# Optimization experiments

Hardware: AMD Instinct MI355X
Metric: run time of the kernel (lower is better)

## Reference

```python
import jax, jax.numpy as jnp
import numpy as np

B, T, H = 4, 2048, 512
HEADS = 8
D = H // HEADS  # head dim = 64


def setup_inputs() -> dict:
    key = jax.random.key(0)
    ks = jax.random.split(key, 5)
    s = 1.0 / np.sqrt(H)
    return {
        "x": jax.random.normal(ks[0], (B, T, H), dtype=jnp.float32),
        "w_qkv": jax.random.uniform(ks[1], (H, 3 * H), dtype=jnp.float32, minval=-s, maxval=s),
        "b_qkv": jax.random.uniform(ks[2], (3 * H,), dtype=jnp.float32, minval=-s, maxval=s),
        "w_proj": jax.random.uniform(ks[3], (H, H), dtype=jnp.float32, minval=-s, maxval=s),
        "b_proj": jax.random.uniform(ks[4], (H,), dtype=jnp.float32, minval=-s, maxval=s),
    }


def reference(x, w_qkv, b_qkv, w_proj, b_proj):
    b, t, h = x.shape
    scale = (h // HEADS) ** (-0.5)
    qkv = (x @ w_qkv + b_qkv).reshape(b, t, 3, HEADS, h // HEADS)
    q, k, v = qkv[:, :, 0], qkv[:, :, 1], qkv[:, :, 2]  # [b,t,heads,d]
    q = q * scale
    scores = jnp.einsum('bthd,bThd->bhtT', q, k)  # [b,heads,t,t]
    weights = jax.nn.softmax(scores, axis=-1)
    attn = jnp.einsum('bhtT,bThd->bthd', weights, v).reshape(b, t, h)
    return attn @ w_proj + b_proj
```

## Files before the change

### kernel.cpp

```cpp
#include <hip/hip_runtime.h>
#include <stdint.h>

typedef unsigned short u16;
typedef __attribute__((ext_vector_type(8))) __bf16 bf16x8;
typedef __attribute__((ext_vector_type(4))) __bf16 bf16x4;
typedef __attribute__((ext_vector_type(4))) float f32x4;
typedef __attribute__((ext_vector_type(2))) unsigned int u32x2;
typedef __attribute__((ext_vector_type(4))) unsigned int u32x4;

#define QSCALE 0.18033688011112042f

__device__ __forceinline__ u16 f2bf(float f) {
    uint32_t u = __builtin_bit_cast(uint32_t, f);
    u = (u + 0x7fffu + ((u >> 16) & 1u)) >> 16;
    return (u16)u;
}
__device__ __forceinline__ float bf2f(u16 h) {
    uint32_t u = ((uint32_t)h) << 16;
    return __builtin_bit_cast(float, u);
}

__device__ __forceinline__ void gl_lds16(const u16* g, u16* l) {
    __builtin_amdgcn_global_load_lds(
        (__attribute__((address_space(1))) uint32_t*)(g),
        (__attribute__((address_space(3))) uint32_t*)(l), 16, 0, 0);
}

__global__ __launch_bounds__(256) void convert_x_k(const float* __restrict__ xf,
                                                   u16* __restrict__ xbf) {
    const size_t v = (size_t)blockIdx.x * 256 + threadIdx.x;
    const f32x4 val = ((const f32x4*)xf)[v];
    u32x2 p;
    p.x = (uint32_t)f2bf(val.x) | ((uint32_t)f2bf(val.y) << 16);
    p.y = (uint32_t)f2bf(val.z) | ((uint32_t)f2bf(val.w) << 16);
    *(u32x2*)&xbf[v * 4] = p;
}

__global__ void transpose_cvt_k(const float* __restrict__ in,
                                u16* __restrict__ out, int R, int C) {
    __shared__ u16 t[64][65];
    const int bx = blockIdx.x << 6, by = blockIdx.y << 6;
    const int tx = threadIdx.x, ty = threadIdx.y;
#pragma unroll
    for (int i = ty; i < 64; i += 8)
        t[i][tx] = f2bf(in[(size_t)(by + i) * C + bx + tx]);
    __syncthreads();
#pragma unroll
    for (int i = ty; i < 64; i += 8) out[(size_t)(bx + i) * R + by + tx] = t[tx][i];
}

template <int EPI>
__global__ __launch_bounds__(256) void gemm_bt_k(
    const u16* __restrict__ A, const u16* __restrict__ Bt,
    const float* __restrict__ bias,
    u16* __restrict__ Qb, u16* __restrict__ Kb, u16* __restrict__ Vt,
    float* __restrict__ OutF) {
    __shared__ u16 lA[128 * 32];
    __shared__ u16 lB[128 * 32];
    const int tid = threadIdx.x;
    const int w = tid >> 6, l = tid & 63, quad = l >> 4, r = l & 15;
    const int tm = blockIdx.x << 7, tn = blockIdx.y << 7;
    const int wm = (w >> 1) << 6, wn = (w & 1) << 6;
    const int srow = l >> 2, sch = (l & 3) << 3;

    f32x4 acc[4][4];
#pragma unroll
    for (int i = 0; i < 4; ++i)
#pragma unroll
        for (int j = 0; j < 4; ++j) acc[i][j] = (f32x4){0.f, 0.f, 0.f, 0.f};

    for (int kk = 0; kk < 512; kk += 32) {
        __syncthreads();
#pragma unroll
        for (int ii = 0; ii < 2; ++ii) {
            const int rowl = w * 32 + ii * 16;
            gl_lds16(A + (size_t)(tm + rowl + srow) * 512 + kk + sch, &lA[rowl * 32]);
            gl_lds16(Bt + (size_t)(tn + rowl + srow) * 512 + kk + sch, &lB[rowl * 32]);
        }
        __syncthreads();
        bf16x8 af[4], bfr[4];
#pragma unroll
        for (int mi = 0; mi < 4; ++mi)
            af[mi] = *(const bf16x8*)&lA[(wm + mi * 16 + r) * 32 + quad * 8];
#pragma unroll
        for (int ni = 0; ni < 4; ++ni)
            bfr[ni] = *(const bf16x8*)&lB[(wn + ni * 16 + r) * 32 + quad * 8];
#pragma unroll
        for (int mi = 0; mi < 4; ++mi)
#pragma unroll
            for (int ni = 0; ni < 4; ++ni)
                acc[mi][ni] = __builtin_amdgcn_mfma_f32_16x16x32_bf16(
                    af[mi], bfr[ni], acc[mi][ni], 0, 0, 0);
    }

#pragma unroll
    for (int ni = 0; ni < 4; ++ni) {
        const int n = tn + wn + ni * 16 + r;
        const float bv = bias[n];
        const int which = n >> 9, head = (n >> 6) & 7, d = n & 63;
#pragma unroll
        for (int mi = 0; mi < 4; ++mi) {
#pragma unroll
            for (int i = 0; i < 4; ++i) {
                const int m = tm + wm + mi * 16 + quad * 4 + i;
                const float v = acc[mi][ni][i] + bv;
                if (EPI == 0) {
                    const int bb = m >> 11, t = m & 2047;
                    const int bh = bb * 8 + head;
                    if (which == 0)
                        Qb[((size_t)(bh * 2048 + t) << 6) + d] = f2bf(v * QSCALE);
                    else if (which == 1)
                        Kb[((size_t)(bh * 2048 + t) << 6) + d] = f2bf(v);
                    else
                        Vt[((size_t)(bh * 64 + d) << 11) + t] = f2bf(v);
                } else {
                    OutF[(size_t)m * 512 + n] = v;
                }
            }
        }
    }
}

__global__ __launch_bounds__(256) void attn_k(
    const u16* __restrict__ Qb, const u16* __restrict__ Kb,
    const u16* __restrict__ Vt, u16* __restrict__ attnb) {
    __shared__ u16 lk[64 * 64];
    __shared__ u16 lv[64 * 64];
    __shared__ u16 lp[4][16 * 72];
    const int tid = threadIdx.x;
    const int w = tid >> 6, l = tid & 63, quad = l >> 4, r = l & 15;
    const int qt = blockIdx.x, bh = blockIdx.y;
    const size_t qbase = (size_t)bh * 2048 + qt * 64;
    const int srl = l >> 3;
    const int sg = (l & 7) ^ srl;

    const bf16x8 qf0 = *(const bf16x8*)&Qb[((qbase + w * 16 + r) << 6) + quad * 8];
    const bf16x8 qf1 = *(const bf16x8*)&Qb[((qbase + w * 16 + r) << 6) + 32 + quad * 8];

    const int rl = r & 7;
    const int rhi = r >> 3;

    const u32x4 onesu = {0x3F803F80u, 0x3F803F80u, 0x3F803F80u, 0x3F803F80u};
    const bf16x8 vones = __builtin_bit_cast(bf16x8, onesu);

    f32x4 o[4];
#pragma unroll
    for (int i = 0; i < 4; ++i) o[i] = (f32x4){0.f, 0.f, 0.f, 0.f};
    f32x4 osum = (f32x4){0.f, 0.f, 0.f, 0.f};

    for (int kv0 = 0; kv0 < 2048; kv0 += 64) {
        __syncthreads();
#pragma unroll
        for (int ii = 0; ii < 2; ++ii) {
            const int chunk = w * 2 + ii;
            gl_lds16(Kb + ((size_t)(bh * 2048 + kv0 + chunk * 8 + srl) << 6) + sg * 8,
                     &lk[chunk * 512]);
            gl_lds16(Vt + (((size_t)(bh * 64 + chunk * 8 + srl)) << 11) + kv0 + sg * 8,
                     &lv[chunk * 512]);
        }
        __syncthreads();

#pragma unroll
        for (int kt = 0; kt < 4; ++kt) {
            const int base = (kt * 2 + rhi) * 512 + rl * 64;
            const bf16x8 a0 = *(const bf16x8*)&lk[base + (quad ^ rl) * 8];
            const bf16x8 a1 = *(const bf16x8*)&lk[base + ((quad ^ rl) ^ 4) * 8];
            f32x4 z = (f32x4){0.f, 0.f, 0.f, 0.f};
            z = __builtin_amdgcn_mfma_f32_16x16x32_bf16(a0, qf0, z, 0, 0, 0);
            z = __builtin_amdgcn_mfma_f32_16x16x32_bf16(a1, qf1, z, 0, 0, 0);
            const uint32_t u0 =
                __builtin_bit_cast(uint32_t, __builtin_amdgcn_exp2f(z[0])) + 0x8000u;
            const uint32_t u1 =
                __builtin_bit_cast(uint32_t, __builtin_amdgcn_exp2f(z[1])) + 0x8000u;
            const uint32_t u2 =
                __builtin_bit_cast(uint32_t, __builtin_amdgcn_exp2f(z[2])) + 0x8000u;
            const uint32_t u3 =
                __builtin_bit_cast(uint32_t, __builtin_amdgcn_exp2f(z[3])) + 0x8000u;
            const uint32_t lo = __builtin_amdgcn_perm(u1, u0, 0x07060302u);
            const uint32_t hi = __builtin_amdgcn_perm(u3, u2, 0x07060302u);
            const uint64_t both = (uint64_t)lo | ((uint64_t)hi << 32);
            *(bf16x4*)&lp[w][r * 72 + kt * 16 + quad * 4] =
                __builtin_bit_cast(bf16x4, both);
        }

        asm volatile("s_waitcnt lgkmcnt(0)" ::: "memory");

#pragma unroll
        for (int h = 0; h < 2; ++h) {
            const bf16x8 ap = *(const bf16x8*)&lp[w][r * 72 + h * 32 + quad * 8];
#pragma unroll
            for (int dt = 0; dt < 4; ++dt) {
                const int baseV = (dt * 2 + rhi) * 512 + rl * 64;
                const bf16x8 bv =
                    *(const bf16x8*)&lv[baseV + ((h * 4 + quad) ^ rl) * 8];
                o[dt] = __builtin_amdgcn_mfma_f32_16x16x32_bf16(ap, bv, o[dt], 0, 0, 0);
            }
            osum = __builtin_amdgcn_mfma_f32_16x16x32_bf16(ap, vones, osum, 0, 0, 0);
        }
    }

    const int bb = bh >> 3, head = bh & 7;
#pragma unroll
    for (int i = 0; i < 4; ++i) {
        const float inv = __builtin_amdgcn_rcpf(osum[i]);
        const int row = bb * 2048 + qt * 64 + w * 16 + quad * 4 + i;
#pragma unroll
        for (int dt = 0; dt < 4; ++dt)
            attnb[(size_t)row * 512 + head * 64 + dt * 16 + r] = f2bf(o[dt][i] * inv);
    }
}

extern "C" void kernel_launch(void* const* d_in, const int* in_sizes, int n_in,
                              void* d_out, int out_size, void* d_ws, size_t ws_size,
                              hipStream_t stream) {
    const float *x = nullptr, *wq = nullptr, *bq = nullptr, *wp = nullptr, *bp = nullptr;
    for (int i = 0; i < n_in; ++i) {
        switch (in_sizes[i]) {
            case 4194304: x  = (const float*)d_in[i]; break;
            case 786432:  wq = (const float*)d_in[i]; break;
            case 1536:    bq = (const float*)d_in[i]; break;
            case 262144:  wp = (const float*)d_in[i]; break;
            case 512:     bp = (const float*)d_in[i]; break;
        }
    }
    if (!x || !wq || !bq || !wp || !bp) {
        x = (const float*)d_in[0]; wq = (const float*)d_in[1];
        bq = (const float*)d_in[2]; wp = (const float*)d_in[3];
        bp = (const float*)d_in[4];
    }
    float* out = (float*)d_out;

    char* ws = (char*)d_ws;
    u16* attnb  = (u16*)(ws + 0);
    u16* wqkvT  = (u16*)(ws + 0);
    u16* Qb     = (u16*)(ws + 8388608);
    u16* wprojT = (u16*)(ws + 8388608);
    u16* Kb     = (u16*)(ws + 16777216);
    u16* Vt     = (u16*)(ws + 25165824);
    u16* xbf    = (u16*)d_out;

    convert_x_k<<<dim3(4096), 256, 0, stream>>>(x, xbf);
    transpose_cvt_k<<<dim3(24, 8), dim3(64, 8), 0, stream>>>(wq, wqkvT, 512, 1536);
    gemm_bt_k<0><<<dim3(64, 12), 256, 0, stream>>>(xbf, wqkvT, bq, Qb, Kb, Vt, nullptr);
    attn_k<<<dim3(32, 32), 256, 0, stream>>>(Qb, Kb, Vt, attnb);
    transpose_cvt_k<<<dim3(8, 8), dim3(64, 8), 0, stream>>>(wp, wprojT, 512, 512);
    gemm_bt_k<1><<<dim3(64, 4), 256, 0, stream>>>(attnb, wprojT, bp, nullptr, nullptr,
                                                  nullptr, out);
}
```

Before: 177.9 us.

## Process two 64-row query tiles per attention block to reuse K/V tiles

Each attention workgroup now handles 128 query rows instead of 64, with each wave holding two sets of Q fragments, accumulators and P buffers. Every K/V tile staged in LDS is used for twice as many MFMAs, which halves global K/V traffic and the number of barriers per unit of work. The cost is more registers and LDS per block, and the grid shrinks from 1024 to 512 blocks, which lowers the number of blocks available to fill the CUs.

Result: no change. 178.0 us (+0.1%).

```diff
diff --git a/kernel.cpp b/kernel.cpp
--- a/kernel.cpp
+++ b/kernel.cpp
@@ -126,16 +126,18 @@
     const u16* __restrict__ Vt, u16* __restrict__ attnb) {
     __shared__ u16 lk[64 * 64];
     __shared__ u16 lv[64 * 64];
-    __shared__ u16 lp[4][16 * 72];
+    __shared__ u16 lp[8][16 * 72];
     const int tid = threadIdx.x;
     const int w = tid >> 6, l = tid & 63, quad = l >> 4, r = l & 15;
     const int qt = blockIdx.x, bh = blockIdx.y;
-    const size_t qbase = (size_t)bh * 2048 + qt * 64;
+    const size_t qbase = (size_t)bh * 2048 + qt * 128;
     const int srl = l >> 3;
     const int sg = (l & 7) ^ srl;
 
-    const bf16x8 qf0 = *(const bf16x8*)&Qb[((qbase + w * 16 + r) << 6) + quad * 8];
-    const bf16x8 qf1 = *(const bf16x8*)&Qb[((qbase + w * 16 + r) << 6) + 32 + quad * 8];
+    const bf16x8 qf0a = *(const bf16x8*)&Qb[((qbase + w * 16 + r) << 6) + quad * 8];
+    const bf16x8 qf1a = *(const bf16x8*)&Qb[((qbase + w * 16 + r) << 6) + 32 + quad * 8];
+    const bf16x8 qf0b = *(const bf16x8*)&Qb[((qbase + 64 + w * 16 + r) << 6) + quad * 8];
+    const bf16x8 qf1b = *(const bf16x8*)&Qb[((qbase + 64 + w * 16 + r) << 6) + 32 + quad * 8];
 
     const int rl = r & 7;
     const int rhi = r >> 3;
@@ -143,10 +145,14 @@
     const u32x4 onesu = {0x3F803F80u, 0x3F803F80u, 0x3F803F80u, 0x3F803F80u};
     const bf16x8 vones = __builtin_bit_cast(bf16x8, onesu);
 
-    f32x4 o[4];
-#pragma unroll
-    for (int i = 0; i < 4; ++i) o[i] = (f32x4){0.f, 0.f, 0.f, 0.f};
-    f32x4 osum = (f32x4){0.f, 0.f, 0.f, 0.f};
+    f32x4 oA[4], oB[4];
+#pragma unroll
+    for (int i = 0; i < 4; ++i) {
+        oA[i] = (f32x4){0.f, 0.f, 0.f, 0.f};
+        oB[i] = (f32x4){0.f, 0.f, 0.f, 0.f};
+    }
+    f32x4 osumA = (f32x4){0.f, 0.f, 0.f, 0.f};
+    f32x4 osumB = (f32x4){0.f, 0.f, 0.f, 0.f};
 
     for (int kv0 = 0; kv0 < 2048; kv0 += 64) {
         __syncthreads();
@@ -165,48 +171,66 @@
             const int base = (kt * 2 + rhi) * 512 + rl * 64;
             const bf16x8 a0 = *(const bf16x8*)&lk[base + (quad ^ rl) * 8];
             const bf16x8 a1 = *(const bf16x8*)&lk[base + ((quad ^ rl) ^ 4) * 8];
-            f32x4 z = (f32x4){0.f, 0.f, 0.f, 0.f};
-            z = __builtin_amdgcn_mfma_f32_16x16x32_bf16(a0, qf0, z, 0, 0, 0);
-            z = __builtin_amdgcn_mfma_f32_16x16x32_bf16(a1, qf1, z, 0, 0, 0);
-            const uint32_t u0 =
-                __builtin_bit_cast(uint32_t, __builtin_amdgcn_exp2f(z[0])) + 0x8000u;
-            const uint32_t u1 =
-                __builtin_bit_cast(uint32_t, __builtin_amdgcn_exp2f(z[1])) + 0x8000u;
-            const uint32_t u2 =
-                __builtin_bit_cast(uint32_t, __builtin_amdgcn_exp2f(z[2])) + 0x8000u;
-            const uint32_t u3 =
-                __builtin_bit_cast(uint32_t, __builtin_amdgcn_exp2f(z[3])) + 0x8000u;
-            const uint32_t lo = __builtin_amdgcn_perm(u1, u0, 0x07060302u);
-            const uint32_t hi = __builtin_amdgcn_perm(u3, u2, 0x07060302u);
-            const uint64_t both = (uint64_t)lo | ((uint64_t)hi << 32);
-            *(bf16x4*)&lp[w][r * 72 + kt * 16 + quad * 4] =
-                __builtin_bit_cast(bf16x4, both);
+            f32x4 za = (f32x4){0.f, 0.f, 0.f, 0.f};
+            f32x4 zb = (f32x4){0.f, 0.f, 0.f, 0.f};
+            za = __builtin_amdgcn_mfma_f32_16x16x32_bf16(a0, qf0a, za, 0, 0, 0);
+            za = __builtin_amdgcn_mfma_f32_16x16x32_bf16(a1, qf1a, za, 0, 0, 0);
+            zb = __builtin_amdgcn_mfma_f32_16x16x32_bf16(a0, qf0b, zb, 0, 0, 0);
+            zb = __builtin_amdgcn_mfma_f32_16x16x32_bf16(a1, qf1b, zb, 0, 0, 0);
+#pragma unroll
+            for (int set = 0; set < 2; ++set) {
+                const f32x4 z = set ? zb : za;
+                const uint32_t u0 =
+                    __builtin_bit_cast(uint32_t, __builtin_amdgcn_exp2f(z[0])) + 0x8000u;
+                const uint32_t u1 =
+                    __builtin_bit_cast(uint32_t, __builtin_amdgcn_exp2f(z[1])) + 0x8000u;
+                const uint32_t u2 =
+                    __builtin_bit_cast(uint32_t, __builtin_amdgcn_exp2f(z[2])) + 0x8000u;
+                const uint32_t u3 =
+                    __builtin_bit_cast(uint32_t, __builtin_amdgcn_exp2f(z[3])) + 0x8000u;
+                const uint32_t lo = __builtin_amdgcn_perm(u1, u0, 0x07060302u);
+                const uint32_t hi = __builtin_amdgcn_perm(u3, u2, 0x07060302u);
+                const uint64_t both = (uint64_t)lo | ((uint64_t)hi << 32);
+                *(bf16x4*)&lp[(w << 1) | set][r * 72 + kt * 16 + quad * 4] =
+                    __builtin_bit_cast(bf16x4, both);
+            }
         }
 
         asm volatile("s_waitcnt lgkmcnt(0)" ::: "memory");
 
 #pragma unroll
         for (int h = 0; h < 2; ++h) {
-            const bf16x8 ap = *(const bf16x8*)&lp[w][r * 72 + h * 32 + quad * 8];
+            const bf16x8 apA = *(const bf16x8*)&lp[w << 1][r * 72 + h * 32 + quad * 8];
+            const bf16x8 apB =
+                *(const bf16x8*)&lp[(w << 1) | 1][r * 72 + h * 32 + quad * 8];
 #pragma unroll
             for (int dt = 0; dt < 4; ++dt) {
                 const int baseV = (dt * 2 + rhi) * 512 + rl * 64;
                 const bf16x8 bv =
                     *(const bf16x8*)&lv[baseV + ((h * 4 + quad) ^ rl) * 8];
-                o[dt] = __builtin_amdgcn_mfma_f32_16x16x32_bf16(ap, bv, o[dt], 0, 0, 0);
+                oA[dt] = __builtin_amdgcn_mfma_f32_16x16x32_bf16(apA, bv, oA[dt], 0, 0, 0);
+                oB[dt] = __builtin_amdgcn_mfma_f32_16x16x32_bf16(apB, bv, oB[dt], 0, 0, 0);
             }
-            osum = __builtin_amdgcn_mfma_f32_16x16x32_bf16(ap, vones, osum, 0, 0, 0);
+            osumA = __builtin_amdgcn_mfma_f32_16x16x32_bf16(apA, vones, osumA, 0, 0, 0);
+            osumB = __builtin_amdgcn_mfma_f32_16x16x32_bf16(apB, vones, osumB, 0, 0, 0);
         }
     }
 
     const int bb = bh >> 3, head = bh & 7;
 #pragma unroll
-    for (int i = 0; i < 4; ++i) {
-        const float inv = __builtin_amdgcn_rcpf(osum[i]);
-        const int row = bb * 2048 + qt * 64 + w * 16 + quad * 4 + i;
-#pragma unroll
-        for (int dt = 0; dt < 4; ++dt)
-            attnb[(size_t)row * 512 + head * 64 + dt * 16 + r] = f2bf(o[dt][i] * inv);
+    for (int set = 0; set < 2; ++set) {
+        const f32x4* o = set ? oB : oA;
+        const f32x4 osum = set ? osumB : osumA;
+#pragma unroll
+        for (int i = 0; i < 4; ++i) {
+            const float inv = __builtin_amdgcn_rcpf(osum[i]);
+            const int row =
+                bb * 2048 + qt * 128 + set * 64 + w * 16 + quad * 4 + i;
+#pragma unroll
+            for (int dt = 0; dt < 4; ++dt)
+                attnb[(size_t)row * 512 + head * 64 + dt * 16 + r] =
+                    f2bf(o[dt][i] * inv);
+        }
     }
 }
 
@@ -242,7 +266,7 @@
     convert_x_k<<<dim3(4096), 256, 0, stream>>>(x, xbf);
     transpose_cvt_k<<<dim3(24, 8), dim3(64, 8), 0, stream>>>(wq, wqkvT, 512, 1536);
     gemm_bt_k<0><<<dim3(64, 12), 256, 0, stream>>>(xbf, wqkvT, bq, Qb, Kb, Vt, nullptr);
-    attn_k<<<dim3(32, 32), 256, 0, stream>>>(Qb, Kb, Vt, attnb);
+    attn_k<<<dim3(16, 32), 256, 0, stream>>>(Qb, Kb, Vt, attnb);
     transpose_cvt_k<<<dim3(8, 8), dim3(64, 8), 0, stream>>>(wp, wprojT, 512, 512);
     gemm_bt_k<1><<<dim3(64, 4), 256, 0, stream>>>(attnb, wprojT, bp, nullptr, nullptr,
                                                   nullptr, out);
```
